# Kernel tuning notes

Hardware: AMD Instinct MI355X
Metric: run time of the kernel (lower is better)

## Reference

```python
import jax, jax.numpy as jnp
import numpy as np

PIXEL_THRESHOLD = 0.4
FRACTION_THRESHOLD = 0.03
NUM_CLASSES = 20
N, H, W = 100, 640, 960
LOGIT_SCALE = 8.0  # makes the instance-axis softmax peaky enough to cross PIXEL_THRESHOLD


def setup_inputs() -> dict:
    key = jax.random.key(0)
    k1, k2, k3 = jax.random.split(key, 3)
    cls_prob = jax.random.uniform(k1, (N,), dtype=jnp.float32)
    mask_prob = jax.random.normal(k2, (N, H, W), dtype=jnp.float32) * LOGIT_SCALE
    cls_idx = jax.random.randint(k3, (N,), 0, NUM_CLASSES)
    return {"cls_prob": cls_prob, "mask_prob": mask_prob, "cls_idx": cls_idx}


def _mask_removal(cls_prob, mask_prob, cls_idx):
    # Sort instances by class confidence, descending (greedy NMS order).
    order = jnp.argsort(-cls_prob)
    cls_prob_s = cls_prob[order]          # [N]
    cls_idx_s = cls_idx[order]            # [N]
    raw_s = mask_prob[order]              # [N,H,W] pre-softmax logits (mask_prob_copy)
    # Per-pixel softmax over the instance axis (permutation-equivariant, so
    # softmax-then-sort == sort-then-softmax as in the original).
    sm = jax.nn.softmax(raw_s, axis=0)    # [N,H,W]

    def step(state, inp):
        panoptic, mask_image = state      # [H,W], [C,H,W]
        smi, rawi, ci = inp
        logit = (smi >= PIXEL_THRESHOLD).astype(rawi.dtype)   # binarized mask [H,W]
        mask_sum = logit.sum()
        curr = mask_image[ci]
        overlap = jnp.sum((curr >= 1.0) & (logit == 1.0)).astype(rawi.dtype) / jnp.maximum(mask_sum, 1.0)
        degenerate = (logit.max() == logit.min()) | (mask_sum == 0.0)
        skip = degenerate | (overlap > FRACTION_THRESHOLD)
        # assign only unclaimed panoptic pixels inside the binarized mask
        assign = (panoptic == 0.0) & (logit == 1.0) & jnp.logical_not(skip)
        keep_mask = jnp.where(assign, rawi, 0.0)              # use_mask_low_constant=False
        panoptic = jnp.where(assign, 1.0, panoptic)
        mask_image = mask_image.at[ci].add(jnp.where(assign, logit, 0.0))
        return (panoptic, mask_image), (keep_mask, jnp.logical_not(skip))

    init = (jnp.zeros((H, W), jnp.float32), jnp.zeros((NUM_CLASSES, H, W), jnp.float32))
    _, (keep_masks, keep_flags) = jax.lax.scan(step, init, (sm, raw_s, cls_idx_s))
    # Fixed-shape outputs: keep_flags marks which (sorted) instances survived;
    # dropped instances have all-zero keep_masks rows.
    return cls_prob_s, keep_masks, cls_idx_s, keep_flags


def reference(cls_prob, mask_prob, cls_idx):
    return _mask_removal(cls_prob, mask_prob, cls_idx)
```

## Files before the change

kernel.cpp:

```cpp
#include <hip/hip_runtime.h>
#include <cstdint>
#include <cstddef>

#define N_INST 100
#define HW (640 * 960)
#define PIX_THR 0.4f
#define FRAC_THR 0.03f
#define EPS_BORDER 5e-5f
#define FLAG_CAP 65536
#define L2E 1.4426950408889634f

#define OUT_MASKS_OFF 100
#define OUT_CLSIDX_OFF (100 + (size_t)N_INST * HW)
#define OUT_FLAGS_OFF (100 + (size_t)N_INST * HW + N_INST)


__global__ __launch_bounds__(256) void k0_init(
    const float* __restrict__ cls_prob,
    const int* __restrict__ cls_idx,
    int* __restrict__ ord,
    int* __restrict__ rank_arr,
    float* __restrict__ out,
    unsigned* __restrict__ mask_sum,
    unsigned* __restrict__ flag_count,
    unsigned* __restrict__ pair_cnt) {
    int t = threadIdx.x;
    if (t < N_INST) {
        float pi = cls_prob[t];
        int rank = 0;
        for (int j = 0; j < N_INST; ++j) {
            float pj = cls_prob[j];
            rank += (pj > pi) || (pj == pi && j < t);
        }
        ord[rank] = t;
        rank_arr[t] = rank;
        out[rank] = pi;
        out[OUT_CLSIDX_OFF + rank] = (float)cls_idx[t];
        mask_sum[t] = 0u;
    }
    if (t == 0) *flag_count = 0u;
    for (int i = t; i < N_INST * N_INST; i += 256)
        pair_cnt[i] = 0u;
}

__global__ __launch_bounds__(256) void k1_main(
    const float* __restrict__ mask,
    const int* __restrict__ rank_arr,
    unsigned* __restrict__ mask_sum,
    unsigned* __restrict__ pair_cnt,
    uint4* __restrict__ pvals,
    unsigned* __restrict__ flag_count,
    unsigned* __restrict__ flag_list) {
    __shared__ int srank[N_INST];
    __shared__ unsigned ssum[N_INST];
    int t = threadIdx.x;
    if (t < N_INST) {
        srank[t] = rank_arr[t];
        ssum[t] = 0u;
    }
    __syncthreads();

    int p0 = (blockIdx.x * 256 + t) * 2;
    const float* base = mask + p0;

    float S[2] = {0.0f, 0.0f};
    float m[2] = {-3.4e38f, -3.4e38f};
    float n[2] = {-3.4e38f, -3.4e38f};
    int ia[2] = {0, 0};
    int ib[2] = {0, 0};

#pragma unroll 10
    for (int i = 0; i < N_INST; ++i) {
        float2 v2 = *(const float2*)(base + (size_t)i * HW);
        float vv[2] = {v2.x, v2.y};
#pragma unroll
        for (int j = 0; j < 2; ++j) {
            float v = vv[j];
            S[j] += exp2f(v * L2E);
            bool gt = v > m[j];
            bool g2 = v > n[j];
            n[j] = fmaxf(n[j], fminf(m[j], v));
            ib[j] = gt ? ia[j] : (g2 ? i : ib[j]);
            ia[j] = gt ? i : ia[j];
            m[j] = fmaxf(m[j], v);
        }
    }

#pragma unroll
    for (int j = 0; j < 2; ++j) {
        int p = p0 + j;
        float e1 = exp2f(m[j] * L2E);
        float e2 = exp2f(n[j] * L2E);
        float t04 = 0.4f * S[j];
        float w = EPS_BORDER * S[j];
        bool q1 = e1 >= t04;
        bool border = (fabsf(e1 - t04) < w) || (q1 && fabsf(e2 - t04) < w);

        unsigned c = 0u;
        float vlo = 0.0f, vhi = 0.0f;
        if (border) {
            unsigned slot = atomicAdd(flag_count, 1u);
            if (slot < FLAG_CAP) flag_list[slot] = (unsigned)p;
        } else if (q1) {
            bool q2 = e2 >= t04;
            int r1 = srank[ia[j]];
            atomicAdd(&ssum[r1], 1u);
            if (q2) {
                int r2 = srank[ib[j]];
                atomicAdd(&ssum[r2], 1u);
                int lo = min(r1, r2), hi = max(r1, r2);
                atomicAdd(&pair_cnt[lo * N_INST + hi], 1u);
                c = (unsigned)(lo + 1) | ((unsigned)(hi + 1) << 8);
                vlo = (r1 < r2) ? m[j] : n[j];
                vhi = (r1 < r2) ? n[j] : m[j];
            } else {
                c = (unsigned)(r1 + 1);
                vlo = m[j];
            }
        }
        pvals[p] = make_uint4(c, __float_as_uint(vlo), __float_as_uint(vhi), 0u);
    }

    __syncthreads();
    if (t < N_INST && ssum[t] != 0u)
        atomicAdd(&mask_sum[t], ssum[t]);
}

__global__ void k1_repair(const float* __restrict__ mask,
                          const int* __restrict__ ord,
                          unsigned* __restrict__ mask_sum,
                          unsigned* __restrict__ pair_cnt,
                          uint4* __restrict__ pvals,
                          const unsigned* __restrict__ flag_count,
                          const unsigned* __restrict__ flag_list) {
    __shared__ int sord[N_INST];
    if (threadIdx.x < N_INST) sord[threadIdx.x] = ord[threadIdx.x];
    __syncthreads();

    unsigned nf = *flag_count;
    if (nf > FLAG_CAP) nf = FLAG_CAP;
    for (unsigned idx = blockIdx.x * blockDim.x + threadIdx.x; idx < nf;
         idx += gridDim.x * blockDim.x) {
        int p = (int)flag_list[idx];
        float v[N_INST];
#pragma unroll
        for (int i = 0; i < N_INST; ++i)
            v[i] = mask[(size_t)sord[i] * HW + p];

        float m = v[0];
        int p1 = 0;
        float m2 = -3.4e38f;
        int p2 = 0;
#pragma unroll
        for (int i = 1; i < N_INST; ++i) {
            if (v[i] > m) { m2 = m; p2 = p1; m = v[i]; p1 = i; }
            else if (v[i] > m2) { m2 = v[i]; p2 = i; }
        }
        float d = 0.0f;
#pragma unroll
        for (int i = 0; i < N_INST; ++i)
            d += expf(v[i] - m);

        float sm1 = 1.0f / d;
        float sm2 = expf(m2 - m) / d;
        bool q1 = (sm1 >= PIX_THR);
        bool q2 = (sm2 >= PIX_THR);
        unsigned c = 0u;
        float vlo = 0.0f, vhi = 0.0f;
        if (q1) {
            atomicAdd(&mask_sum[p1], 1u);
            if (q2) {
                atomicAdd(&mask_sum[p2], 1u);
                int lo = min(p1, p2), hi = max(p1, p2);
                atomicAdd(&pair_cnt[lo * N_INST + hi], 1u);
                c = (unsigned)(lo + 1) | ((unsigned)(hi + 1) << 8);
                vlo = v[lo];
                vhi = v[hi];
            } else {
                c = (unsigned)(p1 + 1);
                vlo = v[p1];
            }
        }
        pvals[p] = make_uint4(c, __float_as_uint(vlo), __float_as_uint(vhi), 0u);
    }
}

__global__ void k2_scan(const unsigned* __restrict__ mask_sum,
                        const unsigned* __restrict__ pair_cnt,
                        const int* __restrict__ ord,
                        const int* __restrict__ cls_idx,
                        int* __restrict__ keep,
                        float* __restrict__ out) {
    __shared__ unsigned spair[N_INST * N_INST];
    __shared__ int scls[N_INST];
    __shared__ unsigned sms[N_INST];
    __shared__ int skeep[N_INST];
    int t = threadIdx.x;
    for (int i = t; i < N_INST * N_INST; i += 256)
        spair[i] = pair_cnt[i];
    if (t < N_INST) {
        scls[t] = cls_idx[ord[t]];
        sms[t] = mask_sum[t];
    }
    __syncthreads();

    for (int b = 0; b < N_INST; ++b) {
        if (t < 64) {
            unsigned cnt = 0u;
            for (int a = t; a < b; a += 64)
                if (skeep[a] && scls[a] == scls[b])
                    cnt += spair[a * N_INST + b];
#pragma unroll
            for (int off = 32; off; off >>= 1)
                cnt += __shfl_down((int)cnt, off);
            if (t == 0) {
                unsigned ms = sms[b];
                float overlap = (float)cnt / fmaxf((float)ms, 1.0f);
                bool degen = (ms == 0u) || (ms == (unsigned)HW);
                bool skip = degen || (overlap > FRAC_THR);
                skeep[b] = skip ? 0 : 1;
            }
        }
        __syncthreads();
    }

    if (t < N_INST) {
        keep[t] = skeep[t];
        out[OUT_FLAGS_OFF + t] = (float)skeep[t];
    }
}

__global__ __launch_bounds__(256) void k3_scatter(
    const uint4* __restrict__ pvals,
    const int* __restrict__ keep,
    float* __restrict__ out) {
    __shared__ int skeep[N_INST];
    if (threadIdx.x < N_INST) skeep[threadIdx.x] = keep[threadIdx.x];
    __syncthreads();

    int p = blockIdx.x * 256 + threadIdx.x;
    uint4 pv = pvals[p];
    unsigned c = pv.x;
    if (c == 0u) return;
    int a = (int)(c & 0xFFu) - 1;
    int b = (int)(c >> 8) - 1;

    int inst;
    float val;
    if (skeep[a]) {
        inst = a;
        val = __uint_as_float(pv.y);
    } else if (b >= 0 && skeep[b]) {
        inst = b;
        val = __uint_as_float(pv.z);
    } else {
        return;
    }
    out[OUT_MASKS_OFF + (size_t)inst * HW + p] = val;
}

extern "C" void kernel_launch(void* const* d_in, const int* in_sizes, int n_in,
                              void* d_out, int out_size, void* d_ws, size_t ws_size,
                              hipStream_t stream) {
    const float* cls_prob = (const float*)d_in[0];
    const float* mask = (const float*)d_in[1];
    const int* cls_idx = (const int*)d_in[2];
    float* out = (float*)d_out;

    char* ws = (char*)d_ws;
    int* ord = (int*)(ws + 0);
    int* rank_arr = (int*)(ws + 512);
    int* keep = (int*)(ws + 1024);
    unsigned* mask_sum = (unsigned*)(ws + 1536);
    unsigned* flag_count = (unsigned*)(ws + 2048);
    unsigned* pair_cnt = (unsigned*)(ws + 4096);
    uint4* pvals = (uint4*)(ws + 65536);
    unsigned* flag_list = (unsigned*)(ws + 65536 + (size_t)HW * 16);

    hipMemsetAsync(d_out, 0, (size_t)out_size * sizeof(float), stream);

    k0_init<<<1, 256, 0, stream>>>(cls_prob, cls_idx, ord, rank_arr, out,
                                   mask_sum, flag_count, pair_cnt);
    k1_main<<<HW / 512, 256, 0, stream>>>(mask, rank_arr, mask_sum, pair_cnt,
                                          pvals, flag_count, flag_list);
    k1_repair<<<16, 256, 0, stream>>>(mask, ord, mask_sum, pair_cnt, pvals,
                                      flag_count, flag_list);
    k2_scan<<<1, 256, 0, stream>>>(mask_sum, pair_cnt, ord, cls_idx, keep, out);
    k3_scatter<<<HW / 256, 256, 0, stream>>>(pvals, keep, out);
}
```

Before: 235.6 us.

## Fuse output zeroing into dense mask writer and widen main pass to float4

The separate memset of the whole output and the sparse scatter kernel are replaced by one dense kernel. For each pixel it writes either the kept value or zero for every instance row, using float4 stores. The main softmax/top-2 pass now handles four pixels per thread with float4 loads and 128-thread blocks. This is meant to remove the extra write pass over the large mask output and to improve load width, at the cost of fewer resident waves per CU in the streaming pass.

```diff
diff --git a/kernel.cpp b/kernel.cpp
--- a/kernel.cpp
+++ b/kernel.cpp
@@ -43,7 +43,7 @@
         pair_cnt[i] = 0u;
 }
 
-__global__ __launch_bounds__(256) void k1_main(
+__global__ __launch_bounds__(128) void k1_main(
     const float* __restrict__ mask,
     const int* __restrict__ rank_arr,
     unsigned* __restrict__ mask_sum,
@@ -60,21 +60,21 @@
     }
     __syncthreads();
 
-    int p0 = (blockIdx.x * 256 + t) * 2;
+    int p0 = (blockIdx.x * 128 + t) * 4;
     const float* base = mask + p0;
 
-    float S[2] = {0.0f, 0.0f};
-    float m[2] = {-3.4e38f, -3.4e38f};
-    float n[2] = {-3.4e38f, -3.4e38f};
-    int ia[2] = {0, 0};
-    int ib[2] = {0, 0};
+    float S[4] = {0.0f, 0.0f, 0.0f, 0.0f};
+    float m[4] = {-3.4e38f, -3.4e38f, -3.4e38f, -3.4e38f};
+    float n[4] = {-3.4e38f, -3.4e38f, -3.4e38f, -3.4e38f};
+    int ia[4] = {0, 0, 0, 0};
+    int ib[4] = {0, 0, 0, 0};
 
 #pragma unroll 10
     for (int i = 0; i < N_INST; ++i) {
-        float2 v2 = *(const float2*)(base + (size_t)i * HW);
-        float vv[2] = {v2.x, v2.y};
-#pragma unroll
-        for (int j = 0; j < 2; ++j) {
+        float4 v4 = *(const float4*)(base + (size_t)i * HW);
+        float vv[4] = {v4.x, v4.y, v4.z, v4.w};
+#pragma unroll
+        for (int j = 0; j < 4; ++j) {
             float v = vv[j];
             S[j] += exp2f(v * L2E);
             bool gt = v > m[j];
@@ -87,7 +87,7 @@
     }
 
 #pragma unroll
-    for (int j = 0; j < 2; ++j) {
+    for (int j = 0; j < 4; ++j) {
         int p = p0 + j;
         float e1 = exp2f(m[j] * L2E);
         float e2 = exp2f(n[j] * L2E);
@@ -230,33 +230,45 @@
     }
 }
 
-__global__ __launch_bounds__(256) void k3_scatter(
+__global__ __launch_bounds__(128) void k3_dense(
     const uint4* __restrict__ pvals,
     const int* __restrict__ keep,
     float* __restrict__ out) {
     __shared__ int skeep[N_INST];
-    if (threadIdx.x < N_INST) skeep[threadIdx.x] = keep[threadIdx.x];
-    __syncthreads();
-
-    int p = blockIdx.x * 256 + threadIdx.x;
-    uint4 pv = pvals[p];
-    unsigned c = pv.x;
-    if (c == 0u) return;
-    int a = (int)(c & 0xFFu) - 1;
-    int b = (int)(c >> 8) - 1;
-
-    int inst;
-    float val;
-    if (skeep[a]) {
-        inst = a;
-        val = __uint_as_float(pv.y);
-    } else if (b >= 0 && skeep[b]) {
-        inst = b;
-        val = __uint_as_float(pv.z);
-    } else {
-        return;
-    }
-    out[OUT_MASKS_OFF + (size_t)inst * HW + p] = val;
+    int t = threadIdx.x;
+    if (t < N_INST) skeep[t] = keep[t];
+    __syncthreads();
+
+    int p0 = (blockIdx.x * 128 + t) * 4;
+
+    int inst[4];
+    float val[4];
+#pragma unroll
+    for (int j = 0; j < 4; ++j) {
+        uint4 pv = pvals[p0 + j];
+        unsigned c = pv.x;
+        int a = (int)(c & 0xFFu) - 1;
+        int b = (int)(c >> 8) - 1;
+        int as = -1;
+        float v = 0.0f;
+        if (a >= 0) {
+            if (skeep[a]) { as = a; v = __uint_as_float(pv.y); }
+            else if (b >= 0 && skeep[b]) { as = b; v = __uint_as_float(pv.z); }
+        }
+        inst[j] = as;
+        val[j] = v;
+    }
+
+    float* dst = out + OUT_MASKS_OFF + p0;
+#pragma unroll 4
+    for (int i = 0; i < N_INST; ++i) {
+        float4 o;
+        o.x = (inst[0] == i) ? val[0] : 0.0f;
+        o.y = (inst[1] == i) ? val[1] : 0.0f;
+        o.z = (inst[2] == i) ? val[2] : 0.0f;
+        o.w = (inst[3] == i) ? val[3] : 0.0f;
+        *(float4*)(dst + (size_t)i * HW) = o;
+    }
 }
 
 extern "C" void kernel_launch(void* const* d_in, const int* in_sizes, int n_in,
@@ -277,14 +289,12 @@
     uint4* pvals = (uint4*)(ws + 65536);
     unsigned* flag_list = (unsigned*)(ws + 65536 + (size_t)HW * 16);
 
-    hipMemsetAsync(d_out, 0, (size_t)out_size * sizeof(float), stream);
-
     k0_init<<<1, 256, 0, stream>>>(cls_prob, cls_idx, ord, rank_arr, out,
                                    mask_sum, flag_count, pair_cnt);
-    k1_main<<<HW / 512, 256, 0, stream>>>(mask, rank_arr, mask_sum, pair_cnt,
+    k1_main<<<HW / 512, 128, 0, stream>>>(mask, rank_arr, mask_sum, pair_cnt,
                                           pvals, flag_count, flag_list);
     k1_repair<<<16, 256, 0, stream>>>(mask, ord, mask_sum, pair_cnt, pvals,
                                       flag_count, flag_list);
     k2_scan<<<1, 256, 0, stream>>>(mask_sum, pair_cnt, ord, cls_idx, keep, out);
-    k3_scatter<<<HW / 256, 256, 0, stream>>>(pvals, keep, out);
-}
+    k3_dense<<<HW / 512, 128, 0, stream>>>(pvals, keep, out);
+}
```

Measured after the change: 278.2 us. 1.18x slower.

## Fuse output zeroing into main pass blocks and widen per-thread pixel loads

Applied to the files above, without the earlier changes.

Removes the separate memset of the whole output and instead assigns extra blocks of the main kernel to zero the masks region with float4 stores, so the zeroing overlaps the streaming reduction over the logits. The main pass also now handles four pixels per thread with float4 loads and 128-thread blocks. The memset no longer covers the first 100 cls_prob slots, the class-index slots or the flags. Correctness relies on k0 and k2 writing those regions themselves, and the zeroing must finish before k3 scatters into the masks.

```diff
diff --git a/kernel.cpp b/kernel.cpp
--- a/kernel.cpp
+++ b/kernel.cpp
@@ -9,6 +9,12 @@
 #define EPS_BORDER 5e-5f
 #define FLAG_CAP 65536
 #define L2E 1.4426950408889634f
+
+#define CB 1200
+#define ZB 480
+#define F4_TOTAL (N_INST * HW / 4)
+#define F4_PER_BLOCK (F4_TOTAL / ZB)
+#define F4_PER_THREAD (F4_PER_BLOCK / 128)
 
 #define OUT_MASKS_OFF 100
 #define OUT_CLSIDX_OFF (100 + (size_t)N_INST * HW)
@@ -43,38 +49,50 @@
         pair_cnt[i] = 0u;
 }
 
-__global__ __launch_bounds__(256) void k1_main(
+__global__ __launch_bounds__(128) void k1_fused(
     const float* __restrict__ mask,
     const int* __restrict__ rank_arr,
     unsigned* __restrict__ mask_sum,
     unsigned* __restrict__ pair_cnt,
     uint4* __restrict__ pvals,
     unsigned* __restrict__ flag_count,
-    unsigned* __restrict__ flag_list) {
+    unsigned* __restrict__ flag_list,
+    float* __restrict__ out) {
+    int t = threadIdx.x;
+
+    if (blockIdx.x >= CB) {
+        int zb = blockIdx.x - CB;
+        float4* dst = (float4*)(out + OUT_MASKS_OFF) + (size_t)zb * F4_PER_BLOCK + t;
+        const float4 z4 = make_float4(0.0f, 0.0f, 0.0f, 0.0f);
+#pragma unroll 10
+        for (int k = 0; k < F4_PER_THREAD; ++k)
+            dst[k * 128] = z4;
+        return;
+    }
+
     __shared__ int srank[N_INST];
     __shared__ unsigned ssum[N_INST];
-    int t = threadIdx.x;
     if (t < N_INST) {
         srank[t] = rank_arr[t];
         ssum[t] = 0u;
     }
     __syncthreads();
 
-    int p0 = (blockIdx.x * 256 + t) * 2;
+    int p0 = (blockIdx.x * 128 + t) * 4;
     const float* base = mask + p0;
 
-    float S[2] = {0.0f, 0.0f};
-    float m[2] = {-3.4e38f, -3.4e38f};
-    float n[2] = {-3.4e38f, -3.4e38f};
-    int ia[2] = {0, 0};
-    int ib[2] = {0, 0};
+    float S[4] = {0.0f, 0.0f, 0.0f, 0.0f};
+    float m[4] = {-3.4e38f, -3.4e38f, -3.4e38f, -3.4e38f};
+    float n[4] = {-3.4e38f, -3.4e38f, -3.4e38f, -3.4e38f};
+    int ia[4] = {0, 0, 0, 0};
+    int ib[4] = {0, 0, 0, 0};
 
 #pragma unroll 10
     for (int i = 0; i < N_INST; ++i) {
-        float2 v2 = *(const float2*)(base + (size_t)i * HW);
-        float vv[2] = {v2.x, v2.y};
-#pragma unroll
-        for (int j = 0; j < 2; ++j) {
+        float4 v4 = *(const float4*)(base + (size_t)i * HW);
+        float vv[4] = {v4.x, v4.y, v4.z, v4.w};
+#pragma unroll
+        for (int j = 0; j < 4; ++j) {
             float v = vv[j];
             S[j] += exp2f(v * L2E);
             bool gt = v > m[j];
@@ -87,7 +105,7 @@
     }
 
 #pragma unroll
-    for (int j = 0; j < 2; ++j) {
+    for (int j = 0; j < 4; ++j) {
         int p = p0 + j;
         float e1 = exp2f(m[j] * L2E);
         float e2 = exp2f(n[j] * L2E);
@@ -277,12 +295,10 @@
     uint4* pvals = (uint4*)(ws + 65536);
     unsigned* flag_list = (unsigned*)(ws + 65536 + (size_t)HW * 16);
 
-    hipMemsetAsync(d_out, 0, (size_t)out_size * sizeof(float), stream);
-
     k0_init<<<1, 256, 0, stream>>>(cls_prob, cls_idx, ord, rank_arr, out,
                                    mask_sum, flag_count, pair_cnt);
-    k1_main<<<HW / 512, 256, 0, stream>>>(mask, rank_arr, mask_sum, pair_cnt,
-                                          pvals, flag_count, flag_list);
+    k1_fused<<<CB + ZB, 128, 0, stream>>>(mask, rank_arr, mask_sum, pair_cnt,
+                                          pvals, flag_count, flag_list, out);
     k1_repair<<<16, 256, 0, stream>>>(mask, ord, mask_sum, pair_cnt, pvals,
                                       flag_count, flag_list);
     k2_scan<<<1, 256, 0, stream>>>(mask_sum, pair_cnt, ord, cls_idx, keep, out);
```

New measurement: 248.5 us. 1.05x slower.
